# Kernel optimization log

Hardware: AMD Instinct MI355X
Metric: run time of the kernel (lower is better)

The kernel has to match this reference:

```python
import jax, jax.numpy as jnp
import numpy as np

B, T, N, D, S, V, H = 8, 256, 32, 128, 8, 32000, 4
CHUNK = 8

def _ln(x, g, b, eps=1e-5):
    m = x.mean(-1, keepdims=True)
    v = ((x - m) ** 2).mean(-1, keepdims=True)
    return (x - m) / jnp.sqrt(v + eps) * g + b

def _gelu(x):
    return jax.nn.gelu(x, approximate=False)

def setup_inputs() -> dict:
    key = jax.random.key(0)
    ks = iter(jax.random.split(key, 64))
    def nrm(shape, scale=0.02):
        return jax.random.normal(next(ks), shape, jnp.float32) * scale
    def brain(din):
        w = jax.random.normal(next(ks), (N, din, D), jnp.float32) / np.sqrt(din)
        return w, jnp.zeros((N, D), jnp.float32)
    inp = {}
    inp['idx'] = jax.random.randint(next(ks), (B, T), 0, V)
    inp['emb'] = nrm((V, D))
    inp['pos_emb'] = nrm((T, D))
    inp['ifc_w'] = nrm((D, D)); inp['ifc_b'] = jnp.zeros((D,))
    inp['ifc_g'] = jnp.ones((D,)); inp['ifc_beta'] = jnp.zeros((D,))
    inp['sproj_w'] = nrm((D, S * D)); inp['sproj_b'] = jnp.zeros((S * D,))
    inp['sgate_w'] = nrm((2 * D, D)); inp['sgate_b'] = jnp.zeros((D,))
    for name, din in [('P', 3 * D), ('D1', 2 * D), ('D2', D), ('A', D), ('G', 2 * D), ('SM', D), ('PR', D)]:
        w, b = brain(din)
        inp[name + '_w'] = w; inp[name + '_b'] = b
    for name in ['cq', 'ck', 'cv', 'co']:
        inp[name + '_w'] = nrm((D, D)); inp[name + '_b'] = jnp.zeros((D,))
    inp['cln_g'] = jnp.ones((D,)); inp['cln_b'] = jnp.zeros((D,))
    inp['sal_w'] = nrm((D, 1)); inp['sal_b'] = jnp.zeros((1,))
    inp['bcast_w'] = nrm((D, D)); inp['bcast_b'] = jnp.zeros((D,))
    inp['wln_g'] = jnp.ones((D,)); inp['wln_b'] = jnp.zeros((D,))
    inp['res_w'] = nrm((D, D)); inp['res_b'] = jnp.zeros((D,))
    inp['out_w'] = nrm((2 * D, D)); inp['out_b'] = jnp.zeros((D,))
    inp['out_bias'] = jnp.zeros((V,))
    inp['ln_g'] = jnp.ones((D,)); inp['ln_b'] = jnp.zeros((D,))
    return inp

def reference(idx, emb, pos_emb, ifc_w, ifc_b, ifc_g, ifc_beta, sproj_w, sproj_b,
              sgate_w, sgate_b, P_w, P_b, D1_w, D1_b, D2_w, D2_b, A_w, A_b, G_w, G_b,
              SM_w, SM_b, PR_w, PR_b, cq_w, cq_b, ck_w, ck_b, cv_w, cv_b, co_w, co_b,
              cln_g, cln_b, sal_w, sal_b, bcast_w, bcast_b, wln_g, wln_b,
              res_w, res_b, out_w, out_b, out_bias, ln_g, ln_b):
    # Embed + interface (eval mode: dropout = identity, no gumbel / training noise)
    raw = emb[idx] + pos_emb[:T][None]  # (B,T,D)
    percepts = _ln(_gelu(raw @ ifc_w + ifc_b), ifc_g, ifc_beta)
    pc = percepts.reshape(B, T // CHUNK, CHUNK, D).transpose(1, 2, 0, 3)  # (nC,CHUNK,B,D)

    def brain_apply(x, w, b):  # per-agent bmm: (B,N,din) x (N,din,D)
        return jnp.einsum('bni,nio->bno', x, w) + b

    def timestep(carry, cur):  # cur: (B,D)
        states, _ = carry
        sensory = (cur @ sproj_w + sproj_b).reshape(B, S, D)
        cs = states[:, :S]
        sg = jax.nn.sigmoid(jnp.concatenate([cs, sensory], -1) @ sgate_w + sgate_b)
        states = jnp.concatenate([sg * cs + (1 - sg) * sensory, states[:, S:]], axis=1)
        sal = (states @ sal_w).squeeze(-1) + sal_b[0]  # (B,N)
        wts = jax.nn.softmax(sal * 5.0, -1)
        workspace = jnp.einsum('bnd,bn->bd', states, wts)
        bcast = _ln(workspace @ bcast_w + bcast_b, wln_g, wln_b)  # (B,D), same for all N
        residual = cur @ res_w + res_b
        proj = _gelu(jnp.concatenate([workspace, residual], -1) @ out_w + out_b)
        logits = proj @ emb.T + out_bias
        return (states, bcast), logits

    def chunk_step(carry, chunk):
        states, prev_pred, has_pred, boredom = carry
        (states, bcast), logits = jax.lax.scan(timestep, (states, jnp.zeros((B, D))), chunk)
        # swarm multi-head cross-attention between agents
        hd = D // H
        def heads(x):
            return x.reshape(B, N, H, hd).transpose(0, 2, 1, 3)
        Q = heads(states @ cq_w + cq_b)
        K = heads(states @ ck_w + ck_b)
        Vv = heads(states @ cv_w + cv_b)
        attn = jax.nn.softmax(Q @ K.transpose(0, 1, 3, 2) / jnp.sqrt(jnp.float32(hd)), -1)
        msg = (attn @ Vv).transpose(0, 2, 1, 3).reshape(B, N, D)
        states = _ln(states + msg @ co_w + co_b, cln_g, cln_b)
        incoming = jnp.broadcast_to(states.mean(1, keepdims=True), (B, N, D))
        # agent_step (eval): surprise gating + EMA boredom + gated recurrent update
        pred_err = ((incoming - prev_pred) ** 2).mean(-1)  # (B,N)
        surprise = jnp.where(has_pred > 0, jax.nn.sigmoid(pred_err * 10.0), 0.0)
        incoming = incoming * (1 + surprise[..., None] * 0.5)
        boredom = 0.99 * boredom + 0.01 * (1 - jax.lax.stop_gradient(surprise).mean(0))
        broadcast = jnp.broadcast_to(bcast[:, None, :], (B, N, D))
        p_in = jnp.concatenate([incoming, broadcast, states], -1)
        perception = _gelu(brain_apply(p_in, P_w, P_b))
        self_pred = brain_apply(states, SM_w, SM_b)
        d_in = jnp.concatenate([perception, self_pred], -1)
        decision = brain_apply(_gelu(brain_apply(d_in, D1_w, D1_b)), D2_w, D2_b)
        g = jax.nn.sigmoid(brain_apply(jnp.concatenate([states, decision], -1), G_w, G_b))
        new_states = _ln(g * decision + (1 - g) * states, ln_g, ln_b)
        prediction = brain_apply(new_states, PR_w, PR_b)
        return (new_states, prediction, jnp.float32(1.0), boredom), logits

    init = (jnp.zeros((B, N, D)), jnp.zeros((B, N, D)), jnp.float32(0.0), jnp.zeros((N,)))
    _, logits = jax.lax.scan(chunk_step, init, pc)  # (nC,CHUNK,B,V)
    return logits.transpose(2, 0, 1, 3).reshape(B, T, V)
```

## Files before the change

### kernel.cpp

```cpp
#include <hip/hip_runtime.h>
#include <hip/hip_bf16.h>

#define B_ 8
#define T_ 256
#define N_ 32
#define D_ 128
#define S_ 8
#define V_ 32000
#define H_ 4
#define HD_ 32
#define NCHUNK 32
#define CH_ 8

__device__ __forceinline__ float gelu_f(float x){
    return 0.5f * x * (1.0f + erff(x * 0.70710678118654752440f));
}
__device__ __forceinline__ float sigm(float x){
    return 1.0f / (1.0f + expf(-x));
}

typedef __attribute__((ext_vector_type(4))) float f32x4v;

__global__ void k_percepts(const int* __restrict__ idx, const float* __restrict__ emb,
                           const float* __restrict__ pos_emb, const float* __restrict__ ifc_w,
                           const float* __restrict__ ifc_b, const float* __restrict__ ifc_g,
                           const float* __restrict__ ifc_beta, float* __restrict__ percepts){
    int r = blockIdx.x;
    int t = r % T_;
    int d = threadIdx.x;
    __shared__ float raw[D_];
    __shared__ float red[D_];
    int tok = idx[r];
    raw[d] = emb[tok*D_ + d] + pos_emb[t*D_ + d];
    __syncthreads();
    float acc = ifc_b[d];
    #pragma unroll 8
    for (int k=0;k<D_;k++) acc += raw[k]*ifc_w[k*D_+d];
    float x = gelu_f(acc);
    red[d] = x; __syncthreads();
    for (int s=64;s>0;s>>=1){ if(d<s) red[d]+=red[d+s]; __syncthreads(); }
    float m = red[0]*(1.0f/D_); __syncthreads();
    float dv = x-m; red[d] = dv*dv; __syncthreads();
    for (int s=64;s>0;s>>=1){ if(d<s) red[d]+=red[d+s]; __syncthreads(); }
    float var = red[0]*(1.0f/D_);
    percepts[r*D_ + d] = dv * (1.0f/sqrtf(var + 1e-5f)) * ifc_g[d] + ifc_beta[d];
}

__global__ void __launch_bounds__(256) k_precomp(const float* __restrict__ percepts,
                          const float* __restrict__ sproj_w, const float* __restrict__ sproj_b,
                          const float* __restrict__ sgate_w,
                          const float* __restrict__ res_w, const float* __restrict__ res_b,
                          const float* __restrict__ out_w,
                          float* __restrict__ sensory, float* __restrict__ sg_sens,
                          float* __restrict__ outres){
    int blk = blockIdx.x;
    int b = blk >> 5, c = blk & 31;
    int tid = threadIdx.x;
    __shared__ float p[CH_][D_];
    __shared__ float sens[CH_][S_*D_];
    __shared__ float resid[CH_][D_];
    int tbase = b*T_ + c*CH_;
    for (int i = tid; i < CH_*D_; i += 256) p[i>>7][i&127] = percepts[(tbase + (i>>7))*D_ + (i&127)];
    __syncthreads();
    for (int q=0;q<4;q++){
        int sd = tid + 256*q;
        float acc[CH_];
        #pragma unroll
        for(int i=0;i<CH_;i++) acc[i] = sproj_b[sd];
        for (int k=0;k<D_;k++){
            float w = sproj_w[k*(S_*D_) + sd];
            #pragma unroll
            for(int i=0;i<CH_;i++) acc[i] += p[i][k]*w;
        }
        #pragma unroll
        for(int i=0;i<CH_;i++){
            sens[i][sd] = acc[i];
            sensory[(size_t)(tbase+i)*(S_*D_) + sd] = acc[i];
        }
    }
    __syncthreads();
    {
        int d = tid & 127, h = tid >> 7;
        float acc[4][S_];
        #pragma unroll
        for(int ii=0;ii<4;ii++)
            #pragma unroll
            for(int s=0;s<S_;s++) acc[ii][s]=0.f;
        for (int k=0;k<D_;k++){
            float w = sgate_w[(D_+k)*D_ + d];
            #pragma unroll
            for(int ii=0;ii<4;ii++){
                int i = h*4+ii;
                #pragma unroll
                for(int s=0;s<S_;s++) acc[ii][s] += sens[i][s*D_+k]*w;
            }
        }
        for(int ii=0;ii<4;ii++){ int i=h*4+ii;
            for(int s=0;s<S_;s++) sg_sens[((size_t)(tbase+i)*S_+s)*D_ + d] = acc[ii][s];
        }
    }
    __syncthreads();
    {
        int d = tid & 127, h = tid>>7;
        float acc[4];
        #pragma unroll
        for(int ii=0;ii<4;ii++) acc[ii]=res_b[d];
        for(int k=0;k<D_;k++){
            float w = res_w[k*D_+d];
            #pragma unroll
            for(int ii=0;ii<4;ii++) acc[ii] += p[h*4+ii][k]*w;
        }
        for(int ii=0;ii<4;ii++) resid[h*4+ii][d]=acc[ii];
    }
    __syncthreads();
    {
        int d = tid & 127, h = tid>>7;
        float acc[4];
        #pragma unroll
        for(int ii=0;ii<4;ii++) acc[ii]=0.f;
        for(int k=0;k<D_;k++){
            float w = out_w[(D_+k)*D_ + d];
            #pragma unroll
            for(int ii=0;ii<4;ii++) acc[ii] += resid[h*4+ii][k]*w;
        }
        for(int ii=0;ii<4;ii++) outres[(size_t)(tbase+h*4+ii)*D_ + d] = acc[ii];
    }
}

#define ST_O   0
#define SGW_O  4096
#define KT_O   20480
#define VT_O   24608
#define QT_O   28736
#define AW_O   32864
#define RED_O  33888
#define SMEM_A 33952

__global__ void __launch_bounds__(1024) k_fused(int c,
        const float* __restrict__ sensory, const float* __restrict__ sg_sens,
        const float* __restrict__ sgate_w, const float* __restrict__ sgate_b,
        const float* __restrict__ sal_w, const float* __restrict__ sal_b,
        const float* __restrict__ out_w, const float* __restrict__ out_b,
        const float* __restrict__ outres,
        const float* __restrict__ bcast_w, const float* __restrict__ bcast_b,
        const float* __restrict__ wln_g, const float* __restrict__ wln_b,
        const float* __restrict__ cq_w, const float* __restrict__ cq_b,
        const float* __restrict__ ck_w, const float* __restrict__ ck_b,
        const float* __restrict__ cv_w, const float* __restrict__ cv_b,
        const float* __restrict__ co_w, const float* __restrict__ co_b,
        const float* __restrict__ cln_g, const float* __restrict__ cln_b,
        const float* __restrict__ states, float* __restrict__ states2,
        float* __restrict__ bcastv, float* __restrict__ meanv,
        float* __restrict__ projb){
    const int b = blockIdx.x;
    const int tid = threadIdx.x;
    __shared__ float smem[SMEM_A];
    float* st  = &smem[ST_O];
    float* sgw = &smem[SGW_O];

    for (int i=tid;i<N_*D_;i+=1024) st[i] = states[b*N_*D_+i];
    {
        const f32x4v* gw = reinterpret_cast<const f32x4v*>(sgate_w);
        f32x4v* lw = reinterpret_cast<f32x4v*>(sgw);
        for (int i=tid;i<D_*D_/4;i+=1024) lw[i] = gw[i];
    }
    __syncthreads();

    {
        float* ns    = &smem[KT_O];
        float* ppart = &smem[VT_O];
        float* wsv   = &smem[QT_O];
        float* salv  = &smem[QT_O+128];
        float* wtsv  = &smem[QT_O+160];
        float* redb  = &smem[QT_O+192];
        const int s = tid >> 7, d = tid & 127;
        for (int step=0; step<CH_; step++){
            const int tg = b*T_ + c*CH_ + step;
            float acc = sg_sens[((size_t)tg*S_+s)*D_+d] + sgate_b[d];
            const float* stp = &st[s*D_];
            #pragma unroll 8
            for (int k=0;k<D_;k++) acc += stp[k]*sgw[k*D_+d];
            float sg = sigm(acc);
            float sv = sensory[((size_t)tg*S_+s)*D_+d];
            ns[tid] = sg*stp[d] + (1.0f-sg)*sv;
            __syncthreads();
            st[tid] = ns[tid];
            __syncthreads();
            if (tid < 512){
                int nn = tid >> 4, l = tid & 15;
                float pa = 0.f;
                #pragma unroll
                for (int j=0;j<8;j++) pa += st[nn*D_ + l + 16*j]*sal_w[l+16*j];
                #pragma unroll
                for (int off=8;off;off>>=1) pa += __shfl_down(pa, off, 16);
                if (l==0) salv[nn] = pa + sal_b[0];
            }
            __syncthreads();
            if (tid < 64){
                float v = (tid<N_)? salv[tid]*5.0f : -1e30f;
                float m = v;
                #pragma unroll
                for (int off=32;off;off>>=1) m = fmaxf(m, __shfl_xor(m, off, 64));
                float e = (tid<N_)? expf(v-m) : 0.f;
                float Z = e;
                #pragma unroll
                for (int off=32;off;off>>=1) Z += __shfl_xor(Z, off, 64);
                if (tid<N_) wtsv[tid] = e/Z;
            }
            __syncthreads();
            if (tid < D_){
                float w = 0.f;
                #pragma unroll 4
                for (int n=0;n<N_;n++) w += wtsv[n]*st[n*D_+tid];
                wsv[tid] = w;
            }
            __syncthreads();
            {
                const int ks = tid >> 7;
                float ap = 0.f;
                #pragma unroll
                for (int k2=0;k2<16;k2++){ int k = ks*16+k2; ap += wsv[k]*out_w[k*D_+d]; }
                ppart[tid] = ap;
            }
            __syncthreads();
            if (tid < D_){
                float a2 = out_b[tid] + outres[(size_t)tg*D_+tid];
                #pragma unroll
                for (int j=0;j<8;j++) a2 += ppart[j*128+tid];
                projb[(size_t)tg*D_+tid] = gelu_f(a2);
            }
            if (step==CH_-1){
                float a3 = 0.f;
                if (tid<D_){
                    a3 = bcast_b[tid];
                    #pragma unroll 8
                    for (int k=0;k<D_;k++) a3 += wsv[k]*bcast_w[k*D_+tid];
                    redb[tid] = a3;
                }
                __syncthreads();
                for (int sh=64;sh;sh>>=1){ if(tid<sh) redb[tid]+=redb[tid+sh]; __syncthreads(); }
                float mb = redb[0]*(1.0f/D_);
                __syncthreads();
                float dvv = a3-mb;
                if (tid<D_) redb[tid] = dvv*dvv;
                __syncthreads();
                for (int sh=64;sh;sh>>=1){ if(tid<sh) redb[tid]+=redb[tid+sh]; __syncthreads(); }
                float vb = redb[0]*(1.0f/D_);
                if (tid<D_) bcastv[b*D_+tid] = dvv*(1.0f/sqrtf(vb+1e-5f))*wln_g[tid]+wln_b[tid];
            }
            __syncthreads();
        }
    }

    {
        const int g = tid >> 7, d2 = tid & 127;
        float aK[4], aV[4], aQ[4];
        #pragma unroll
        for (int q=0;q<4;q++){ aK[q]=ck_b[d2]; aV[q]=cv_b[d2]; aQ[q]=cq_b[d2]; }
        #pragma unroll 4
        for (int k=0;k<D_;k++){
            float wq = cq_w[k*D_+d2];
            float wk = ck_w[k*D_+d2];
            float wv = cv_w[k*D_+d2];
            #pragma unroll
            for (int q=0;q<4;q++){
                float x = st[(q*8+g)*D_+k];
                aQ[q] += x*wq; aK[q] += x*wk; aV[q] += x*wv;
            }
        }
        #pragma unroll
        for (int q=0;q<4;q++){
            smem[KT_O+(q*8+g)*129+d2] = aK[q];
            smem[VT_O+(q*8+g)*129+d2] = aV[q];
            smem[QT_O+(q*8+g)*129+d2] = aQ[q];
        }
        __syncthreads();
        for (int ni=0;ni<4;ni++){
            const int n = ni*8+g;
            {
                const int h = d2>>5, m = d2&31;
                float sdot = 0.f;
                #pragma unroll
                for (int j=0;j<HD_;j++) sdot += smem[QT_O+n*129+h*32+j]*smem[KT_O+m*129+h*32+j];
                sdot *= 0.17677669529663687f;
                float mx = sdot;
                #pragma unroll
                for (int off=16;off;off>>=1) mx = fmaxf(mx, __shfl_xor(mx, off, 32));
                float e = expf(sdot-mx);
                float Z = e;
                #pragma unroll
                for (int off=16;off;off>>=1) Z += __shfl_xor(Z, off, 32);
                smem[AW_O+g*128+h*32+m] = e/Z;
            }
            __syncthreads();
            {
                const int h2 = d2>>5;
                float mm = 0.f;
                #pragma unroll 8
                for (int m2=0;m2<N_;m2++) mm += smem[AW_O+g*128+h2*32+m2]*smem[VT_O+m2*129+d2];
                smem[QT_O+n*129+d2] = mm;
            }
            __syncthreads();
        }
        float acc2[4];
        #pragma unroll
        for (int q=0;q<4;q++) acc2[q] = co_b[d2];
        #pragma unroll 4
        for (int k=0;k<D_;k++){
            float w = co_w[k*D_+d2];
            #pragma unroll
            for (int q=0;q<4;q++) acc2[q] += smem[QT_O+(q*8+g)*129+k]*w;
        }
        for (int q=0;q<4;q++){
            const int n = q*8+g;
            float x = st[n*D_+d2] + acc2[q];
            float s1 = x, s2 = x*x;
            #pragma unroll
            for (int off=32;off;off>>=1){
                s1 += __shfl_xor(s1, off, 64);
                s2 += __shfl_xor(s2, off, 64);
            }
            if ((d2&63)==0){
                smem[RED_O + g*4 + (d2>>6)*2    ] = s1;
                smem[RED_O + g*4 + (d2>>6)*2 + 1] = s2;
            }
            __syncthreads();
            s1 = smem[RED_O+g*4]   + smem[RED_O+g*4+2];
            s2 = smem[RED_O+g*4+1] + smem[RED_O+g*4+3];
            float mn  = s1*(1.0f/D_);
            float var = s2*(1.0f/D_) - mn*mn;
            float st2v = (x-mn)*(1.0f/sqrtf(var+1e-5f))*cln_g[d2]+cln_b[d2];
            states2[((size_t)b*N_+n)*D_+d2] = st2v;
            st[n*D_+d2] = st2v;
            __syncthreads();
        }
        if (tid < D_){
            float sm_ = 0.f;
            #pragma unroll 4
            for (int n2=0;n2<N_;n2++) sm_ += st[n2*D_+tid];
            meanv[b*D_+tid] = sm_*(1.0f/N_);
        }
    }
}

__global__ void __launch_bounds__(512) k_brains(int c,
        const float* __restrict__ states2, const float* __restrict__ bcast,
        const float* __restrict__ meanv,
        const float* __restrict__ P_w, const float* __restrict__ P_b,
        const float* __restrict__ D1_w, const float* __restrict__ D1_b,
        const float* __restrict__ D2_w, const float* __restrict__ D2_b,
        const float* __restrict__ G_w, const float* __restrict__ G_b,
        const float* __restrict__ SM_w, const float* __restrict__ SM_b,
        const float* __restrict__ PR_w, const float* __restrict__ PR_b,
        const float* __restrict__ ln_g, const float* __restrict__ ln_b,
        float* __restrict__ states, float* __restrict__ prediction){
    int blk = blockIdx.x;
    int x8 = blk & 7, qq = blk >> 3;
    int n = x8 + 8*(qq & 3), b = qq >> 2;
    int tid = threadIdx.x, d = tid & 127, h = tid >> 7;
    __shared__ float pin[3*D_];
    __shared__ float strow[D_];
    __shared__ float part[4*D_];
    __shared__ float din[2*D_];
    __shared__ float gin[2*D_];
    __shared__ float dec[D_], nsv[D_];
    __shared__ float red[512];
    const size_t rowb = ((size_t)b*N_+n)*D_;
    float inc = meanv[b*D_+d];
    if (tid < D_) strow[d] = states2[rowb+d];
    float pr = prediction[rowb+d];
    float diff = inc - pr;
    red[tid] = (h==0)? diff*diff : 0.f;
    __syncthreads();
    for (int sh=256;sh;sh>>=1){ if(tid<sh) red[tid]+=red[tid+sh]; __syncthreads(); }
    float pe = red[0]*(1.0f/D_);
    float surprise = (c>0)? sigm(pe*10.0f) : 0.0f;
    float scale = 1.0f + 0.5f*surprise;
    __syncthreads();
    if (h==0){
        pin[d]      = inc*scale;
        pin[D_+d]   = bcast[b*D_+d];
        pin[2*D_+d] = strow[d];
    }
    __syncthreads();
    {
        const float* Wn = P_w + ((size_t)n*384 + h*96)*D_ + d;
        float a=0;
        #pragma unroll 4
        for (int k=0;k<96;k++) a += pin[h*96+k]*Wn[(size_t)k*D_];
        part[h*128+d]=a;
        __syncthreads();
        if (h==0) din[d] = gelu_f(part[d]+part[128+d]+part[256+d]+part[384+d]+P_b[n*D_+d]);
        __syncthreads();
    }
    {
        const float* Wn = SM_w + ((size_t)n*128 + h*32)*D_ + d;
        float a=0;
        #pragma unroll 4
        for (int k=0;k<32;k++) a += strow[h*32+k]*Wn[(size_t)k*D_];
        part[h*128+d]=a;
        __syncthreads();
        if (h==0) din[D_+d] = part[d]+part[128+d]+part[256+d]+part[384+d]+SM_b[n*D_+d];
        __syncthreads();
    }
    {
        const float* Wn = D1_w + ((size_t)n*256 + h*64)*D_ + d;
        float a=0;
        #pragma unroll 4
        for (int k=0;k<64;k++) a += din[h*64+k]*Wn[(size_t)k*D_];
        part[h*128+d]=a;
        __syncthreads();
        if (h==0) pin[d] = gelu_f(part[d]+part[128+d]+part[256+d]+part[384+d]+D1_b[n*D_+d]);
        __syncthreads();
    }
    {
        const float* Wn = D2_w + ((size_t)n*128 + h*32)*D_ + d;
        float a=0;
        #pragma unroll 4
        for (int k=0;k<32;k++) a += pin[h*32+k]*Wn[(size_t)k*D_];
        part[h*128+d]=a;
        __syncthreads();
        if (h==0){ float v = part[d]+part[128+d]+part[256+d]+part[384+d]+D2_b[n*D_+d];
                   dec[d]=v; gin[d]=strow[d]; gin[D_+d]=v; }
        __syncthreads();
    }
    {
        const float* Wn = G_w + ((size_t)n*256 + h*64)*D_ + d;
        float a=0;
        #pragma unroll 4
        for (int k=0;k<64;k++) a += gin[h*64+k]*Wn[(size_t)k*D_];
        part[h*128+d]=a;
        __syncthreads();
    }
    float gg=0.f, pre=0.f;
    if (h==0){
        gg = sigm(part[d]+part[128+d]+part[256+d]+part[384+d]+G_b[n*D_+d]);
        pre = gg*dec[d] + (1.0f-gg)*strow[d];
    }
    red[tid] = (h==0)? pre : 0.f;
    __syncthreads();
    for (int sh=256;sh;sh>>=1){ if(tid<sh) red[tid]+=red[tid+sh]; __syncthreads(); }
    float mn = red[0]*(1.0f/D_);
    __syncthreads();
    float dv2 = pre-mn;
    red[tid] = (h==0)? dv2*dv2 : 0.f;
    __syncthreads();
    for (int sh=256;sh;sh>>=1){ if(tid<sh) red[tid]+=red[tid+sh]; __syncthreads(); }
    float var = red[0]*(1.0f/D_);
    __syncthreads();
    if (h==0){
        float nv = dv2*(1.0f/sqrtf(var+1e-5f))*ln_g[d]+ln_b[d];
        nsv[d]=nv;
        states[rowb+d]=nv;
    }
    __syncthreads();
    {
        const float* Wn = PR_w + ((size_t)n*128 + h*32)*D_ + d;
        float a=0;
        #pragma unroll 4
        for (int k=0;k<32;k++) a += nsv[h*32+k]*Wn[(size_t)k*D_];
        part[h*128+d]=a;
        __syncthreads();
        if (h==0) prediction[rowb+d] = part[d]+part[128+d]+part[256+d]+part[384+d]+PR_b[n*D_+d];
    }
}

__global__ void k_tobf16(const float* __restrict__ src, __hip_bfloat16* __restrict__ dst, int nelem){
    int i = blockIdx.x*256 + threadIdx.x;
    int stride = gridDim.x*256;
    for (; i<nelem; i+=stride) dst[i] = __float2bfloat16(src[i]);
}

typedef __attribute__((ext_vector_type(8))) short short8;
typedef __attribute__((ext_vector_type(4))) float f32x4;

__global__ void __launch_bounds__(256) k_gemm(const __hip_bfloat16* __restrict__ A,
                       const __hip_bfloat16* __restrict__ Bv,
                       const float* __restrict__ out_bias,
                       float* __restrict__ out){
    int vblk = blockIdx.x;
    int mblk = blockIdx.y;
    int tid = threadIdx.x;
    int wave = tid >> 6, lane = tid & 63;
    int l16 = lane & 15, quad = lane >> 4;
    int mrow = mblk*64 + wave*16 + l16;
    f32x4 acc[16];
    #pragma unroll
    for (int j=0;j<16;j++){ f32x4 z = {0.f,0.f,0.f,0.f}; acc[j]=z; }
    short8 afr[4];
    const short* Ap = reinterpret_cast<const short*>(A);
    #pragma unroll
    for (int ks=0;ks<4;ks++)
        afr[ks] = *reinterpret_cast<const short8*>(Ap + mrow*128 + ks*32 + quad*8);
    const short* Bp = reinterpret_cast<const short*>(Bv);
    int vcolbase = vblk*256;
    #pragma unroll
    for (int jj=0;jj<16;jj++){
        int v = vcolbase + jj*16 + l16;
        #pragma unroll
        for (int ks=0;ks<4;ks++){
            short8 bfr = *reinterpret_cast<const short8*>(Bp + (size_t)v*128 + ks*32 + quad*8);
            acc[jj] = __builtin_amdgcn_mfma_f32_16x16x32_bf16(afr[ks], bfr, acc[jj], 0,0,0);
        }
    }
    int mbase = mblk*64 + wave*16 + quad*4;
    #pragma unroll
    for (int jj=0;jj<16;jj++){
        int v = vcolbase + jj*16 + l16;
        float bias = out_bias[v];
        #pragma unroll
        for (int r=0;r<4;r++){
            out[(size_t)(mbase+r)*V_ + v] = acc[jj][r] + bias;
        }
    }
}

extern "C" void kernel_launch(void* const* d_in, const int* in_sizes, int n_in,
                              void* d_out, int out_size, void* d_ws, size_t ws_size,
                              hipStream_t stream){
    (void)in_sizes; (void)n_in; (void)out_size; (void)ws_size;
    const int*   idx      = (const int*)  d_in[0];
    const float* emb      = (const float*)d_in[1];
    const float* pos_emb  = (const float*)d_in[2];
    const float* ifc_w    = (const float*)d_in[3];
    const float* ifc_b    = (const float*)d_in[4];
    const float* ifc_g    = (const float*)d_in[5];
    const float* ifc_beta = (const float*)d_in[6];
    const float* sproj_w  = (const float*)d_in[7];
    const float* sproj_b  = (const float*)d_in[8];
    const float* sgate_w  = (const float*)d_in[9];
    const float* sgate_b  = (const float*)d_in[10];
    const float* P_w  = (const float*)d_in[11];
    const float* P_b  = (const float*)d_in[12];
    const float* D1_w = (const float*)d_in[13];
    const float* D1_b = (const float*)d_in[14];
    const float* D2_w = (const float*)d_in[15];
    const float* D2_b = (const float*)d_in[16];
    const float* G_w  = (const float*)d_in[19];
    const float* G_b  = (const float*)d_in[20];
    const float* SM_w = (const float*)d_in[21];
    const float* SM_b = (const float*)d_in[22];
    const float* PR_w = (const float*)d_in[23];
    const float* PR_b = (const float*)d_in[24];
    const float* cq_w = (const float*)d_in[25];
    const float* cq_b = (const float*)d_in[26];
    const float* ck_w = (const float*)d_in[27];
    const float* ck_b = (const float*)d_in[28];
    const float* cv_w = (const float*)d_in[29];
    const float* cv_b = (const float*)d_in[30];
    const float* co_w = (const float*)d_in[31];
    const float* co_b = (const float*)d_in[32];
    const float* cln_g = (const float*)d_in[33];
    const float* cln_b = (const float*)d_in[34];
    const float* sal_w = (const float*)d_in[35];
    const float* sal_b = (const float*)d_in[36];
    const float* bcast_w = (const float*)d_in[37];
    const float* bcast_b = (const float*)d_in[38];
    const float* wln_g = (const float*)d_in[39];
    const float* wln_b = (const float*)d_in[40];
    const float* res_w = (const float*)d_in[41];
    const float* res_b = (const float*)d_in[42];
    const float* out_w = (const float*)d_in[43];
    const float* out_b = (const float*)d_in[44];
    const float* out_bias = (const float*)d_in[45];
    const float* ln_g = (const float*)d_in[46];
    const float* ln_b = (const float*)d_in[47];

    float* ws = (float*)d_ws;
    float* states     = ws + 0;
    float* prediction = ws + 32768;
    float* states2    = ws + 65536;
    float* bcastv     = ws + 98304;
    float* meanv      = ws + 99328;
    float* percepts   = ws + 197632;
    float* sensory    = ws + 459776;
    float* sg_sens    = ws + 2556928;
    float* outresb    = ws + 4654080;
    float* projb      = ws + 4916224;
    __hip_bfloat16* proj_bf = (__hip_bfloat16*)(ws + 5178368);
    __hip_bfloat16* emb_bf  = (__hip_bfloat16*)(ws + 5309440);

    hipMemsetAsync(states, 0, 2*32768*sizeof(float), stream);

    k_tobf16<<<512,256,0,stream>>>(emb, emb_bf, V_*D_);
    k_percepts<<<B_*T_,128,0,stream>>>(idx, emb, pos_emb, ifc_w, ifc_b, ifc_g, ifc_beta, percepts);
    k_precomp<<<256,256,0,stream>>>(percepts, sproj_w, sproj_b, sgate_w, res_w, res_b, out_w,
                                    sensory, sg_sens, outresb);
    for (int c=0;c<NCHUNK;c++){
        k_fused<<<B_,1024,0,stream>>>(c, sensory, sg_sens, sgate_w, sgate_b, sal_w, sal_b,
                                      out_w, out_b, outresb, bcast_w, bcast_b, wln_g, wln_b,
                                      cq_w,cq_b, ck_w,ck_b, cv_w,cv_b, co_w,co_b, cln_g,cln_b,
                                      states, states2, bcastv, meanv, projb);
        k_brains<<<256,512,0,stream>>>(c, states2, bcastv, meanv, P_w,P_b,D1_w,D1_b,D2_w,D2_b,
                                       G_w,G_b,SM_w,SM_b,PR_w,PR_b, ln_g,ln_b,
                                       states, prediction);
    }
    k_tobf16<<<256,256,0,stream>>>(projb, proj_bf, B_*T_*D_);
    k_gemm<<<dim3(125,32),256,0,stream>>>(proj_bf, emb_bf, out_bias, (float*)d_out);
}
```

Baseline: 4.299 ms.

## Cut barriers in sequential chunk loop and widen brains kernel to 1024 threads

In the fused per-chunk kernel, salience for the untouched slot rows 8..31 is computed once before the step loop, and each step only recomputes rows 0..7. The output projection and broadcast layernorm are deferred until after the loop, using stored per-step workspace vectors, which removes several barriers and tree reductions from the serial step chain. Next-step sensory inputs are prefetched into registers. The brains kernel now uses 1024 threads, runs the P and SM matmuls concurrently, splits K more finely, and replaces shared-memory tree reductions with wave shuffles, trading more threads per block for fewer serial syncs.

```diff
diff --git a/kernel.cpp b/kernel.cpp
--- a/kernel.cpp
+++ b/kernel.cpp
@@ -157,6 +157,11 @@
     __shared__ float smem[SMEM_A];
     float* st  = &smem[ST_O];
     float* sgw = &smem[SGW_O];
+    float* ns   = &smem[KT_O];
+    float* salv = &smem[QT_O+128];
+    float* wtsv = &smem[QT_O+160];
+    float* wall = &smem[AW_O];
+    float* red  = &smem[RED_O];
 
     for (int i=tid;i<N_*D_;i+=1024) st[i] = states[b*N_*D_+i];
     {
@@ -166,31 +171,42 @@
     }
     __syncthreads();
 
-    {
-        float* ns    = &smem[KT_O];
-        float* ppart = &smem[VT_O];
-        float* wsv   = &smem[QT_O];
-        float* salv  = &smem[QT_O+128];
-        float* wtsv  = &smem[QT_O+160];
-        float* redb  = &smem[QT_O+192];
+    if (tid < 384){
+        int nn = 8 + (tid>>4), l = tid&15;
+        float pa = 0.f;
+        #pragma unroll
+        for (int j=0;j<8;j++) pa += st[nn*D_ + l + 16*j]*sal_w[l+16*j];
+        #pragma unroll
+        for (int off=8;off;off>>=1) pa += __shfl_down(pa, off, 16);
+        if (l==0) salv[nn] = pa + sal_b[0];
+    }
+    __syncthreads();
+
+    {
         const int s = tid >> 7, d = tid & 127;
+        const float sgb = sgate_b[d];
+        const float* stp = &st[s*D_];
+        size_t gbase = ((size_t)(b*T_ + c*CH_)*S_ + s)*D_ + d;
+        float sgs = sg_sens[gbase], sv = sensory[gbase];
         for (int step=0; step<CH_; step++){
-            const int tg = b*T_ + c*CH_ + step;
-            float acc = sg_sens[((size_t)tg*S_+s)*D_+d] + sgate_b[d];
-            const float* stp = &st[s*D_];
+            float sgs_n=0.f, sv_n=0.f;
+            if (step < CH_-1){
+                sgs_n = sg_sens[gbase + (size_t)(step+1)*(S_*D_)];
+                sv_n  = sensory[gbase + (size_t)(step+1)*(S_*D_)];
+            }
+            float acc = 0.f;
             #pragma unroll 8
             for (int k=0;k<D_;k++) acc += stp[k]*sgw[k*D_+d];
+            acc += sgs + sgb;
             float sg = sigm(acc);
-            float sv = sensory[((size_t)tg*S_+s)*D_+d];
             ns[tid] = sg*stp[d] + (1.0f-sg)*sv;
             __syncthreads();
             st[tid] = ns[tid];
-            __syncthreads();
-            if (tid < 512){
-                int nn = tid >> 4, l = tid & 15;
+            if (tid < 128){
+                int nn = tid>>4, l = tid&15;
                 float pa = 0.f;
                 #pragma unroll
-                for (int j=0;j<8;j++) pa += st[nn*D_ + l + 16*j]*sal_w[l+16*j];
+                for (int j=0;j<8;j++) pa += ns[nn*D_ + l + 16*j]*sal_w[l+16*j];
                 #pragma unroll
                 for (int off=8;off;off>>=1) pa += __shfl_down(pa, off, 16);
                 if (l==0) salv[nn] = pa + sal_b[0];
@@ -212,44 +228,38 @@
                 float w = 0.f;
                 #pragma unroll 4
                 for (int n=0;n<N_;n++) w += wtsv[n]*st[n*D_+tid];
-                wsv[tid] = w;
-            }
-            __syncthreads();
-            {
-                const int ks = tid >> 7;
-                float ap = 0.f;
-                #pragma unroll
-                for (int k2=0;k2<16;k2++){ int k = ks*16+k2; ap += wsv[k]*out_w[k*D_+d]; }
-                ppart[tid] = ap;
-            }
-            __syncthreads();
-            if (tid < D_){
-                float a2 = out_b[tid] + outres[(size_t)tg*D_+tid];
-                #pragma unroll
-                for (int j=0;j<8;j++) a2 += ppart[j*128+tid];
-                projb[(size_t)tg*D_+tid] = gelu_f(a2);
-            }
-            if (step==CH_-1){
-                float a3 = 0.f;
-                if (tid<D_){
-                    a3 = bcast_b[tid];
-                    #pragma unroll 8
-                    for (int k=0;k<D_;k++) a3 += wsv[k]*bcast_w[k*D_+tid];
-                    redb[tid] = a3;
-                }
-                __syncthreads();
-                for (int sh=64;sh;sh>>=1){ if(tid<sh) redb[tid]+=redb[tid+sh]; __syncthreads(); }
-                float mb = redb[0]*(1.0f/D_);
-                __syncthreads();
-                float dvv = a3-mb;
-                if (tid<D_) redb[tid] = dvv*dvv;
-                __syncthreads();
-                for (int sh=64;sh;sh>>=1){ if(tid<sh) redb[tid]+=redb[tid+sh]; __syncthreads(); }
-                float vb = redb[0]*(1.0f/D_);
-                if (tid<D_) bcastv[b*D_+tid] = dvv*(1.0f/sqrtf(vb+1e-5f))*wln_g[tid]+wln_b[tid];
-            }
-            __syncthreads();
-        }
+                wall[step*D_+tid] = w;
+            }
+            __syncthreads();
+            sgs = sgs_n; sv = sv_n;
+        }
+    }
+
+    {
+        const int stp8 = tid >> 7, dd = tid & 127;
+        const int tg = b*T_ + c*CH_ + stp8;
+        float a2 = out_b[dd] + outres[(size_t)tg*D_+dd];
+        const float* wsp = &wall[stp8*D_];
+        #pragma unroll 8
+        for (int k=0;k<D_;k++) a2 += wsp[k]*out_w[k*D_+dd];
+        projb[(size_t)tg*D_+dd] = gelu_f(a2);
+    }
+    float a3 = 0.f;
+    if (tid < D_){
+        a3 = bcast_b[tid];
+        #pragma unroll 8
+        for (int k=0;k<D_;k++) a3 += wall[7*D_+k]*bcast_w[k*D_+tid];
+        float s1 = a3, s2 = a3*a3;
+        #pragma unroll
+        for (int off=32;off;off>>=1){ s1 += __shfl_xor(s1,off,64); s2 += __shfl_xor(s2,off,64); }
+        if ((tid&63)==0){ red[(tid>>6)*2]=s1; red[(tid>>6)*2+1]=s2; }
+    }
+    __syncthreads();
+    if (tid < D_){
+        float s1 = red[0]+red[2], s2 = red[1]+red[3];
+        float mb = s1*(1.0f/D_);
+        float vb = s2*(1.0f/D_) - mb*mb;
+        bcastv[b*D_+tid] = (a3-mb)*(1.0f/sqrtf(vb+1e-5f))*wln_g[tid]+wln_b[tid];
     }
 
     {
@@ -343,7 +353,7 @@
     }
 }
 
-__global__ void __launch_bounds__(512) k_brains(int c,
+__global__ void __launch_bounds__(1024) k_brains(int c,
         const float* __restrict__ states2, const float* __restrict__ bcast,
         const float* __restrict__ meanv,
         const float* __restrict__ P_w, const float* __restrict__ P_b,
@@ -358,110 +368,121 @@
     int x8 = blk & 7, qq = blk >> 3;
     int n = x8 + 8*(qq & 3), b = qq >> 2;
     int tid = threadIdx.x, d = tid & 127, h = tid >> 7;
-    __shared__ float pin[3*D_];
-    __shared__ float strow[D_];
-    __shared__ float part[4*D_];
+    __shared__ float strow[D_], incv[D_], bcv[D_];
     __shared__ float din[2*D_];
-    __shared__ float gin[2*D_];
-    __shared__ float dec[D_], nsv[D_];
-    __shared__ float red[512];
+    __shared__ float h1v[D_], dec[D_], nsv[D_];
+    __shared__ float part[1024];
+    __shared__ float red[8];
     const size_t rowb = ((size_t)b*N_+n)*D_;
-    float inc = meanv[b*D_+d];
-    if (tid < D_) strow[d] = states2[rowb+d];
-    float pr = prediction[rowb+d];
-    float diff = inc - pr;
-    red[tid] = (h==0)? diff*diff : 0.f;
-    __syncthreads();
-    for (int sh=256;sh;sh>>=1){ if(tid<sh) red[tid]+=red[tid+sh]; __syncthreads(); }
-    float pe = red[0]*(1.0f/D_);
-    float surprise = (c>0)? sigm(pe*10.0f) : 0.0f;
-    float scale = 1.0f + 0.5f*surprise;
-    __syncthreads();
     if (h==0){
-        pin[d]      = inc*scale;
-        pin[D_+d]   = bcast[b*D_+d];
-        pin[2*D_+d] = strow[d];
-    }
-    __syncthreads();
-    {
-        const float* Wn = P_w + ((size_t)n*384 + h*96)*D_ + d;
+        float sv = states2[rowb+d]; strow[d]=sv;
+        float iv = meanv[b*D_+d];   incv[d]=iv;
+        float pr = prediction[rowb+d];
+        float df = iv - pr;
+        float s1 = df*df;
+        #pragma unroll
+        for (int off=32;off;off>>=1) s1 += __shfl_xor(s1, off, 64);
+        if ((tid&63)==0) red[tid>>6] = s1;
+    } else if (h==1){
+        bcv[d] = bcast[b*D_+d];
+    }
+    __syncthreads();
+    float pe = (red[0]+red[1])*(1.0f/D_);
+    float scale = (c>0)? (1.0f + 0.5f*sigm(pe*10.0f)) : 1.0f;
+    {
+        float a = 0.f;
+        if (h < 6){
+            int src = h >> 1;
+            const float* xv = (src==0)? incv : (src==1)? bcv : strow;
+            int k0 = (h&1)*64;
+            const float* Wn = P_w + ((size_t)n*384 + src*128 + k0)*D_ + d;
+            #pragma unroll 4
+            for (int k=0;k<64;k++) a += xv[k0+k]*Wn[(size_t)k*D_];
+        } else {
+            int k0 = (h&1)*64;
+            const float* Wn = SM_w + ((size_t)n*128 + k0)*D_ + d;
+            #pragma unroll 4
+            for (int k=0;k<64;k++) a += strow[k0+k]*Wn[(size_t)k*D_];
+        }
+        part[tid] = a;
+    }
+    __syncthreads();
+    if (h==0){
+        float v = scale*(part[d]+part[128+d]) + part[256+d]+part[384+d]+part[512+d]+part[640+d] + P_b[n*D_+d];
+        din[d] = gelu_f(v);
+    } else if (h==1){
+        din[D_+d] = part[768+d]+part[896+d] + SM_b[n*D_+d];
+    }
+    __syncthreads();
+    {
+        const float* Wn = D1_w + ((size_t)n*256 + h*32)*D_ + d;
         float a=0;
         #pragma unroll 4
-        for (int k=0;k<96;k++) a += pin[h*96+k]*Wn[(size_t)k*D_];
-        part[h*128+d]=a;
-        __syncthreads();
-        if (h==0) din[d] = gelu_f(part[d]+part[128+d]+part[256+d]+part[384+d]+P_b[n*D_+d]);
-        __syncthreads();
-    }
-    {
-        const float* Wn = SM_w + ((size_t)n*128 + h*32)*D_ + d;
+        for (int k=0;k<32;k++) a += din[h*32+k]*Wn[(size_t)k*D_];
+        part[tid]=a;
+    }
+    __syncthreads();
+    if (h==0){
+        float v = part[d]+part[128+d]+part[256+d]+part[384+d]+part[512+d]+part[640+d]+part[768+d]+part[896+d] + D1_b[n*D_+d];
+        h1v[d] = gelu_f(v);
+    }
+    __syncthreads();
+    {
+        const float* Wn = D2_w + ((size_t)n*128 + h*16)*D_ + d;
         float a=0;
-        #pragma unroll 4
-        for (int k=0;k<32;k++) a += strow[h*32+k]*Wn[(size_t)k*D_];
-        part[h*128+d]=a;
-        __syncthreads();
-        if (h==0) din[D_+d] = part[d]+part[128+d]+part[256+d]+part[384+d]+SM_b[n*D_+d];
-        __syncthreads();
-    }
-    {
-        const float* Wn = D1_w + ((size_t)n*256 + h*64)*D_ + d;
+        #pragma unroll
+        for (int k=0;k<16;k++) a += h1v[h*16+k]*Wn[(size_t)k*D_];
+        part[tid]=a;
+    }
+    __syncthreads();
+    if (h==0){
+        dec[d] = part[d]+part[128+d]+part[256+d]+part[384+d]+part[512+d]+part[640+d]+part[768+d]+part[896+d] + D2_b[n*D_+d];
+    }
+    __syncthreads();
+    {
         float a=0;
-        #pragma unroll 4
-        for (int k=0;k<64;k++) a += din[h*64+k]*Wn[(size_t)k*D_];
-        part[h*128+d]=a;
-        __syncthreads();
-        if (h==0) pin[d] = gelu_f(part[d]+part[128+d]+part[256+d]+part[384+d]+D1_b[n*D_+d]);
-        __syncthreads();
-    }
-    {
-        const float* Wn = D2_w + ((size_t)n*128 + h*32)*D_ + d;
-        float a=0;
-        #pragma unroll 4
-        for (int k=0;k<32;k++) a += pin[h*32+k]*Wn[(size_t)k*D_];
-        part[h*128+d]=a;
-        __syncthreads();
-        if (h==0){ float v = part[d]+part[128+d]+part[256+d]+part[384+d]+D2_b[n*D_+d];
-                   dec[d]=v; gin[d]=strow[d]; gin[D_+d]=v; }
-        __syncthreads();
-    }
-    {
-        const float* Wn = G_w + ((size_t)n*256 + h*64)*D_ + d;
-        float a=0;
-        #pragma unroll 4
-        for (int k=0;k<64;k++) a += gin[h*64+k]*Wn[(size_t)k*D_];
-        part[h*128+d]=a;
-        __syncthreads();
-    }
-    float gg=0.f, pre=0.f;
+        if (h < 4){
+            const float* Wn = G_w + ((size_t)n*256 + h*32)*D_ + d;
+            #pragma unroll 4
+            for (int k=0;k<32;k++) a += strow[h*32+k]*Wn[(size_t)k*D_];
+        } else {
+            const float* Wn = G_w + ((size_t)n*256 + 128 + (h-4)*32)*D_ + d;
+            #pragma unroll 4
+            for (int k=0;k<32;k++) a += dec[(h-4)*32+k]*Wn[(size_t)k*D_];
+        }
+        part[tid]=a;
+    }
+    __syncthreads();
     if (h==0){
-        gg = sigm(part[d]+part[128+d]+part[256+d]+part[384+d]+G_b[n*D_+d]);
-        pre = gg*dec[d] + (1.0f-gg)*strow[d];
-    }
-    red[tid] = (h==0)? pre : 0.f;
-    __syncthreads();
-    for (int sh=256;sh;sh>>=1){ if(tid<sh) red[tid]+=red[tid+sh]; __syncthreads(); }
-    float mn = red[0]*(1.0f/D_);
-    __syncthreads();
-    float dv2 = pre-mn;
-    red[tid] = (h==0)? dv2*dv2 : 0.f;
-    __syncthreads();
-    for (int sh=256;sh;sh>>=1){ if(tid<sh) red[tid]+=red[tid+sh]; __syncthreads(); }
-    float var = red[0]*(1.0f/D_);
+        float gg = sigm(part[d]+part[128+d]+part[256+d]+part[384+d]+part[512+d]+part[640+d]+part[768+d]+part[896+d] + G_b[n*D_+d]);
+        float pre = gg*dec[d] + (1.0f-gg)*strow[d];
+        nsv[d] = pre;
+        float s1 = pre, s2 = pre*pre;
+        #pragma unroll
+        for (int off=32;off;off>>=1){ s1 += __shfl_xor(s1, off, 64); s2 += __shfl_xor(s2, off, 64); }
+        if ((tid&63)==0){ red[(tid>>6)*2]=s1; red[(tid>>6)*2+1]=s2; }
+    }
     __syncthreads();
     if (h==0){
-        float nv = dv2*(1.0f/sqrtf(var+1e-5f))*ln_g[d]+ln_b[d];
+        float s1 = red[0]+red[2], s2 = red[1]+red[3];
+        float mn = s1*(1.0f/D_);
+        float var = s2*(1.0f/D_) - mn*mn;
+        float pre = nsv[d];
+        float nv = (pre-mn)*(1.0f/sqrtf(var+1e-5f))*ln_g[d]+ln_b[d];
         nsv[d]=nv;
         states[rowb+d]=nv;
     }
     __syncthreads();
     {
-        const float* Wn = PR_w + ((size_t)n*128 + h*32)*D_ + d;
+        const float* Wn = PR_w + ((size_t)n*128 + h*16)*D_ + d;
         float a=0;
-        #pragma unroll 4
-        for (int k=0;k<32;k++) a += nsv[h*32+k]*Wn[(size_t)k*D_];
-        part[h*128+d]=a;
-        __syncthreads();
-        if (h==0) prediction[rowb+d] = part[d]+part[128+d]+part[256+d]+part[384+d]+PR_b[n*D_+d];
+        #pragma unroll
+        for (int k=0;k<16;k++) a += nsv[h*16+k]*Wn[(size_t)k*D_];
+        part[tid]=a;
+    }
+    __syncthreads();
+    if (h==0){
+        prediction[rowb+d] = part[d]+part[128+d]+part[256+d]+part[384+d]+part[512+d]+part[640+d]+part[768+d]+part[896+d] + PR_b[n*D_+d];
     }
 }
 
@@ -591,9 +612,9 @@
                                       out_w, out_b, outresb, bcast_w, bcast_b, wln_g, wln_b,
                                       cq_w,cq_b, ck_w,ck_b, cv_w,cv_b, co_w,co_b, cln_g,cln_b,
                                       states, states2, bcastv, meanv, projb);
-        k_brains<<<256,512,0,stream>>>(c, states2, bcastv, meanv, P_w,P_b,D1_w,D1_b,D2_w,D2_b,
-                                       G_w,G_b,SM_w,SM_b,PR_w,PR_b, ln_g,ln_b,
-                                       states, prediction);
+        k_brains<<<256,1024,0,stream>>>(c, states2, bcastv, meanv, P_w,P_b,D1_w,D1_b,D2_w,D2_b,
+                                        G_w,G_b,SM_w,SM_b,PR_w,PR_b, ln_g,ln_b,
+                                        states, prediction);
     }
     k_tobf16<<<256,256,0,stream>>>(projb, proj_bf, B_*T_*D_);
     k_gemm<<<dim3(125,32),256,0,stream>>>(proj_bf, emb_bf, out_bias, (float*)d_out);
```

Result: faster. 3.653 ms (-15.0%).
